# Kernel optimization log

Measured on AMD Instinct MI355X. Metric: run time of the kernel, lower is better.

## Reference

```python
import jax, jax.numpy as jnp
import numpy as np

SIGMA = 1.0
B, M, D = 32, 4, 196608  # groups, matrix_size, flattened feature dim (3*256*256)


def _mmd_kernel_mean(x, y, w):
    # x, y: [B, m, D] float32; w: [B]
    # Faithful to kernel_fn: dist = sqrt(clamp(sum((x-y)^2), 1e-12)) / D / sigma
    # Pairwise squared distances via gram expansion (avoids materializing [B,m,m,D]).
    xn = jnp.sum(x * x, axis=-1)                     # [B, m]
    yn = jnp.sum(y * y, axis=-1)                     # [B, m]
    xy = jnp.einsum('bid,bjd->bij', x, y)            # [B, m, m]
    d2 = jnp.maximum(xn[:, :, None] + yn[:, None, :] - 2.0 * xy, 1e-12)
    denom = float(D) if D > 0 else 1.0
    sigma = max(float(SIGMA), 1e-6)
    dist = jnp.sqrt(d2) / denom / sigma              # [B, m, m]
    expo = jnp.clip(-dist * w[:, None, None], -1e6, 0.0)
    k = jnp.nan_to_num(jnp.exp(expo), nan=0.0, posinf=0.0, neginf=0.0)
    return jnp.nan_to_num(jnp.mean(k, axis=(1, 2)), nan=0.0)  # [B]


def setup_inputs() -> dict:
    key = jax.random.key(0)
    k1, k2, k3, k4 = jax.random.split(key, 4)
    return {
        'f_st': jax.random.normal(k1, (B, M, D), dtype=jnp.float32),
        'f_sr': jax.random.normal(k2, (B, M, D), dtype=jnp.float32),
        'wt': jax.random.uniform(k3, (B,), dtype=jnp.float32),
        'wtout': jax.random.uniform(k4, (B,), dtype=jnp.float32),
    }


def reference(f_st, f_sr, wt, wtout):
    f_st = f_st.astype(jnp.float32)
    f_sr = f_sr.astype(jnp.float32)
    inter_sample = _mmd_kernel_mean(f_st, f_st, wt)
    inter_gt = _mmd_kernel_mean(f_sr, f_sr, wt)
    cross = _mmd_kernel_mean(f_st, f_sr, wt)
    loss_raw = jnp.nan_to_num(inter_sample + inter_gt - 2.0 * cross, nan=0.0)
    loss = jnp.nan_to_num(wtout * loss_raw, nan=0.0)
    return jnp.mean(loss)
```

## Files before the change

kernel.cpp:

```cpp
#include <hip/hip_runtime.h>


constexpr int NB = 32;
constexpr int MM = 4;
constexpr int DD = 196608;
constexpr int D4 = DD / 4;
constexpr int BPG = 24;
constexpr int NTHREADS = 256;
constexpr int TB = 128;
constexpr int CHUNK4 = D4 / BPG;
constexpr int NITER = CHUNK4 / TB;
constexpr int NBUF = 3;
constexpr int NPAIR = 18;
constexpr int NACC = 36;

__device__ __forceinline__ void gl_lds16(const float4* gsrc, float4* lds_dst) {
    __builtin_amdgcn_global_load_lds(
        (const __attribute__((address_space(1))) void*)gsrc,
        (__attribute__((address_space(3))) void*)lds_dst,
        16, 0, 0);
}

__device__ __forceinline__ float dot4(const float4& a, const float4& b) {
    return a.x * b.x + a.y * b.y + a.z * b.z + a.w * b.w;
}

__global__ __launch_bounds__(NTHREADS) void mmd_partial_kernel(
    const float* __restrict__ st, const float* __restrict__ sr,
    float* __restrict__ partial)
{
    __shared__ float4 buf[NBUF][8][TB];
    __shared__ float red[4][NPAIR];

    const int b    = blockIdx.x / BPG;
    const int blk  = blockIdx.x % BPG;
    const int c0   = blk * CHUNK4;
    const int tid  = threadIdx.x;
    const int wave = tid >> 6;
    const int lane = tid & 63;
    const int col  = tid & (TB - 1);
    const int set  = wave >> 1;

    const float4* stb = reinterpret_cast<const float4*>(st) + (size_t)b * MM * D4;
    const float4* srb = reinterpret_cast<const float4*>(sr) + (size_t)b * MM * D4;

    const int r0 = 2 * wave;
    const float4* g0 = (r0 < 4 ? stb + (size_t)r0 * D4
                                : srb + (size_t)(r0 - 4) * D4) + c0 + lane;
    const float4* g1 = (r0 + 1 < 4 ? stb + (size_t)(r0 + 1) * D4
                                    : srb + (size_t)(r0 - 3) * D4) + c0 + lane;

    auto stage = [&](int s) {
        const int m   = s % NBUF;
        const int off = s * TB;
        gl_lds16(g0 + off,      &buf[m][r0][0]);
        gl_lds16(g0 + off + 64, &buf[m][r0][64]);
        gl_lds16(g1 + off,      &buf[m][r0 + 1][0]);
        gl_lds16(g1 + off + 64, &buf[m][r0 + 1][64]);
    };

    float acc[NPAIR];
#pragma unroll
    for (int k = 0; k < NPAIR; ++k) acc[k] = 0.0f;

    stage(0);
    stage(1);

#pragma unroll
    for (int t = 0; t < NITER; ++t) {
        asm volatile("s_waitcnt lgkmcnt(0)" ::: "memory");
        if (t == NITER - 1) asm volatile("s_waitcnt vmcnt(0)" ::: "memory");
        else                asm volatile("s_waitcnt vmcnt(4)" ::: "memory");
        __builtin_amdgcn_s_barrier();
        if (t + 2 < NITER) stage(t + 2);

        const int m = t % NBUF;
        float4 x[8];
#pragma unroll
        for (int r = 0; r < 8; ++r) x[r] = buf[m][r][col];

        if (set == 0) {
            int a = 0;
#pragma unroll
            for (int i = 0; i < MM; ++i)
#pragma unroll
                for (int j = i; j < MM; ++j) { acc[a] += dot4(x[i], x[j]); ++a; }
#pragma unroll
            for (int i = 0; i < 2; ++i)
#pragma unroll
                for (int j = 0; j < MM; ++j) { acc[a] += dot4(x[i], x[4 + j]); ++a; }
        } else {
            int a = 0;
#pragma unroll
            for (int i = 0; i < MM; ++i)
#pragma unroll
                for (int j = i; j < MM; ++j) { acc[a] += dot4(x[4 + i], x[4 + j]); ++a; }
#pragma unroll
            for (int i = 2; i < 4; ++i)
#pragma unroll
                for (int j = 0; j < MM; ++j) { acc[a] += dot4(x[i], x[4 + j]); ++a; }
        }
    }

#pragma unroll
    for (int k = 0; k < NPAIR; ++k) {
        float v = acc[k];
        for (int off = 32; off > 0; off >>= 1) v += __shfl_down(v, off, 64);
        acc[k] = v;
    }
    if (lane == 0) {
#pragma unroll
        for (int k = 0; k < NPAIR; ++k) red[wave][k] = acc[k];
    }
    __syncthreads();

    if (tid < NACC) {
        const int k = tid;
        float v;
        if (k < 10)       v = red[0][k]      + red[1][k];
        else if (k < 20)  v = red[2][k - 10] + red[3][k - 10];
        else if (k < 28)  v = red[0][10 + (k - 20)] + red[1][10 + (k - 20)];
        else              v = red[2][10 + (k - 28)] + red[3][10 + (k - 28)];
        partial[(size_t)blockIdx.x * NACC + k] = v;
    }
}

__global__ __launch_bounds__(1024) void mmd_final_kernel(
    const float* __restrict__ partial, const float* __restrict__ wt,
    const float* __restrict__ wtout, float* __restrict__ out)
{
    __shared__ float acc_s[NB][NACC];
    for (int p = threadIdx.x; p < NB * NACC; p += 1024) {
        const int b = p / NACC;
        const int k = p % NACC;
        float s = 0.0f;
        for (int blk = 0; blk < BPG; ++blk)
            s += partial[((size_t)b * BPG + blk) * NACC + k];
        acc_s[b][k] = s;
    }
    __syncthreads();

    __shared__ float lds[NB];
    const int b = threadIdx.x;
    if (b < NB) {
        const float* a = acc_s[b];
        float ss[MM][MM], rr[MM][MM], sg[MM][MM];
        {
            int k = 0;
            for (int i = 0; i < MM; ++i)
                for (int j = i; j < MM; ++j) { ss[i][j] = a[k]; ss[j][i] = a[k]; ++k; }
            for (int i = 0; i < MM; ++i)
                for (int j = i; j < MM; ++j) { rr[i][j] = a[k]; rr[j][i] = a[k]; ++k; }
            for (int i = 0; i < MM; ++i)
                for (int j = 0; j < MM; ++j) { sg[i][j] = a[k]; ++k; }
        }

        const float w    = wt[b];
        const float invD = 1.0f / (float)DD;
        auto kv = [&](float d2) -> float {
            d2 = fmaxf(d2, 1e-12f);
            float dist = sqrtf(d2) * invD;
            float e = -dist * w;
            e = fminf(fmaxf(e, -1e6f), 0.0f);
            return expf(e);
        };

        float mss = 0.0f, mrr = 0.0f, msr = 0.0f;
        for (int i = 0; i < MM; ++i) {
            for (int j = 0; j < MM; ++j) {
                mss += kv(ss[i][i] + ss[j][j] - 2.0f * ss[i][j]);
                mrr += kv(rr[i][i] + rr[j][j] - 2.0f * rr[i][j]);
                msr += kv(ss[i][i] + rr[j][j] - 2.0f * sg[i][j]);
            }
        }
        const float inv16 = 1.0f / 16.0f;
        float loss_raw = mss * inv16 + mrr * inv16 - 2.0f * (msr * inv16);
        lds[b] = wtout[b] * loss_raw;
    }
    __syncthreads();
    if (threadIdx.x == 0) {
        float s = 0.0f;
        for (int i = 0; i < NB; ++i) s += lds[i];
        out[0] = s / (float)NB;
    }
}

extern "C" void kernel_launch(void* const* d_in, const int* in_sizes, int n_in,
                              void* d_out, int out_size, void* d_ws, size_t ws_size,
                              hipStream_t stream) {
    const float* f_st  = (const float*)d_in[0];
    const float* f_sr  = (const float*)d_in[1];
    const float* wt    = (const float*)d_in[2];
    const float* wtout = (const float*)d_in[3];
    float* out     = (float*)d_out;
    float* partial = (float*)d_ws;

    mmd_partial_kernel<<<NB * BPG, NTHREADS, 0, stream>>>(f_st, f_sr, partial);
    mmd_final_kernel<<<1, 1024, 0, stream>>>(partial, wt, wtout, out);
}
```

Before: 43.21 us.

## Fuse final reduction via last-block atomics, double grid, rebalance per-wave work

Merges the partial and final kernels into one launch. Per-group atomic counters let the last finishing block of each group reduce its partials, and a global counter lets the last group write the output. The grid grows to 48 blocks per group with a 64-wide tile, and work is repartitioned so each wave owns a distinct Gram sub-block: st-st, sr-sr, or half of the cross terms. The goal is to remove the second kernel launch, its serialized tail and the redundant LDS reads. The cost is an extra memset launch, atomic traffic, and a per-wave work imbalance of 10 vs 8 dot products.

```diff
diff --git a/kernel.cpp b/kernel.cpp
--- a/kernel.cpp
+++ b/kernel.cpp
@@ -5,14 +5,19 @@
 constexpr int MM = 4;
 constexpr int DD = 196608;
 constexpr int D4 = DD / 4;
-constexpr int BPG = 24;
+constexpr int BPG = 48;
+constexpr int NBLOCKS = NB * BPG;
 constexpr int NTHREADS = 256;
-constexpr int TB = 128;
+constexpr int TB = 64;
 constexpr int CHUNK4 = D4 / BPG;
 constexpr int NITER = CHUNK4 / TB;
 constexpr int NBUF = 3;
-constexpr int NPAIR = 18;
 constexpr int NACC = 36;
+
+constexpr size_t PART_BYTES = (size_t)NBLOCKS * NACC * 4;
+constexpr size_t GCNT_OFF   = PART_BYTES;
+constexpr size_t FCNT_OFF   = GCNT_OFF + 128;
+constexpr size_t GLOSS_OFF  = GCNT_OFF + 256;
 
 __device__ __forceinline__ void gl_lds16(const float4* gsrc, float4* lds_dst) {
     __builtin_amdgcn_global_load_lds(
@@ -25,12 +30,24 @@
     return a.x * b.x + a.y * b.y + a.z * b.z + a.w * b.w;
 }
 
-__global__ __launch_bounds__(NTHREADS) void mmd_partial_kernel(
+__device__ __forceinline__ void st_agent(float* p, float v) {
+    __hip_atomic_store(p, v, __ATOMIC_RELAXED, __HIP_MEMORY_SCOPE_AGENT);
+}
+__device__ __forceinline__ float ld_agent(const float* p) {
+    return __hip_atomic_load(p, __ATOMIC_RELAXED, __HIP_MEMORY_SCOPE_AGENT);
+}
+
+__global__ __launch_bounds__(NTHREADS, 6) void mmd_fused_kernel(
     const float* __restrict__ st, const float* __restrict__ sr,
-    float* __restrict__ partial)
+    const float* __restrict__ wt, const float* __restrict__ wtout,
+    float* __restrict__ partial, int* __restrict__ gcnt,
+    int* __restrict__ fcnt, float* __restrict__ gloss,
+    float* __restrict__ out)
 {
     __shared__ float4 buf[NBUF][8][TB];
-    __shared__ float red[4][NPAIR];
+    __shared__ float red[4][10];
+    __shared__ float sgrp[NACC];
+    __shared__ int s_flag;
 
     const int b    = blockIdx.x / BPG;
     const int blk  = blockIdx.x % BPG;
@@ -38,8 +55,6 @@
     const int tid  = threadIdx.x;
     const int wave = tid >> 6;
     const int lane = tid & 63;
-    const int col  = tid & (TB - 1);
-    const int set  = wave >> 1;
 
     const float4* stb = reinterpret_cast<const float4*>(st) + (size_t)b * MM * D4;
     const float4* srb = reinterpret_cast<const float4*>(sr) + (size_t)b * MM * D4;
@@ -51,17 +66,14 @@
                                     : srb + (size_t)(r0 - 3) * D4) + c0 + lane;
 
     auto stage = [&](int s) {
-        const int m   = s % NBUF;
-        const int off = s * TB;
-        gl_lds16(g0 + off,      &buf[m][r0][0]);
-        gl_lds16(g0 + off + 64, &buf[m][r0][64]);
-        gl_lds16(g1 + off,      &buf[m][r0 + 1][0]);
-        gl_lds16(g1 + off + 64, &buf[m][r0 + 1][64]);
+        const int m = s % NBUF;
+        gl_lds16(g0 + s * TB, &buf[m][r0][0]);
+        gl_lds16(g1 + s * TB, &buf[m][r0 + 1][0]);
     };
 
-    float acc[NPAIR];
-#pragma unroll
-    for (int k = 0; k < NPAIR; ++k) acc[k] = 0.0f;
+    float acc[10];
+#pragma unroll
+    for (int k = 0; k < 10; ++k) acc[k] = 0.0f;
 
     stage(0);
     stage(1);
@@ -70,80 +82,86 @@
     for (int t = 0; t < NITER; ++t) {
         asm volatile("s_waitcnt lgkmcnt(0)" ::: "memory");
         if (t == NITER - 1) asm volatile("s_waitcnt vmcnt(0)" ::: "memory");
-        else                asm volatile("s_waitcnt vmcnt(4)" ::: "memory");
+        else                asm volatile("s_waitcnt vmcnt(2)" ::: "memory");
         __builtin_amdgcn_s_barrier();
         if (t + 2 < NITER) stage(t + 2);
 
         const int m = t % NBUF;
-        float4 x[8];
-#pragma unroll
-        for (int r = 0; r < 8; ++r) x[r] = buf[m][r][col];
-
-        if (set == 0) {
+        if (wave == 0) {
+            float4 x[4];
+#pragma unroll
+            for (int r = 0; r < 4; ++r) x[r] = buf[m][r][lane];
             int a = 0;
 #pragma unroll
             for (int i = 0; i < MM; ++i)
 #pragma unroll
                 for (int j = i; j < MM; ++j) { acc[a] += dot4(x[i], x[j]); ++a; }
+        } else if (wave == 1) {
+            float4 x[4];
+#pragma unroll
+            for (int r = 0; r < 4; ++r) x[r] = buf[m][4 + r][lane];
+            int a = 0;
+#pragma unroll
+            for (int i = 0; i < MM; ++i)
+#pragma unroll
+                for (int j = i; j < MM; ++j) { acc[a] += dot4(x[i], x[j]); ++a; }
+        } else {
+            const int ib = (wave == 2) ? 0 : 2;
+            float4 xi[2], y[4];
+            xi[0] = buf[m][ib][lane];
+            xi[1] = buf[m][ib + 1][lane];
+#pragma unroll
+            for (int j = 0; j < 4; ++j) y[j] = buf[m][4 + j][lane];
+            int a = 0;
 #pragma unroll
             for (int i = 0; i < 2; ++i)
 #pragma unroll
-                for (int j = 0; j < MM; ++j) { acc[a] += dot4(x[i], x[4 + j]); ++a; }
-        } else {
-            int a = 0;
-#pragma unroll
-            for (int i = 0; i < MM; ++i)
-#pragma unroll
-                for (int j = i; j < MM; ++j) { acc[a] += dot4(x[4 + i], x[4 + j]); ++a; }
-#pragma unroll
-            for (int i = 2; i < 4; ++i)
-#pragma unroll
-                for (int j = 0; j < MM; ++j) { acc[a] += dot4(x[i], x[4 + j]); ++a; }
-        }
-    }
-
-#pragma unroll
-    for (int k = 0; k < NPAIR; ++k) {
+                for (int j = 0; j < 4; ++j) { acc[a] += dot4(xi[i], y[j]); ++a; }
+        }
+    }
+
+#pragma unroll
+    for (int k = 0; k < 10; ++k) {
         float v = acc[k];
         for (int off = 32; off > 0; off >>= 1) v += __shfl_down(v, off, 64);
         acc[k] = v;
     }
     if (lane == 0) {
 #pragma unroll
-        for (int k = 0; k < NPAIR; ++k) red[wave][k] = acc[k];
+        for (int k = 0; k < 10; ++k) red[wave][k] = acc[k];
     }
     __syncthreads();
 
     if (tid < NACC) {
         const int k = tid;
         float v;
-        if (k < 10)       v = red[0][k]      + red[1][k];
-        else if (k < 20)  v = red[2][k - 10] + red[3][k - 10];
-        else if (k < 28)  v = red[0][10 + (k - 20)] + red[1][10 + (k - 20)];
-        else              v = red[2][10 + (k - 28)] + red[3][10 + (k - 28)];
-        partial[(size_t)blockIdx.x * NACC + k] = v;
-    }
-}
-
-__global__ __launch_bounds__(1024) void mmd_final_kernel(
-    const float* __restrict__ partial, const float* __restrict__ wt,
-    const float* __restrict__ wtout, float* __restrict__ out)
-{
-    __shared__ float acc_s[NB][NACC];
-    for (int p = threadIdx.x; p < NB * NACC; p += 1024) {
-        const int b = p / NACC;
-        const int k = p % NACC;
+        if (k < 10)      v = red[0][k];
+        else if (k < 20) v = red[1][k - 10];
+        else if (k < 28) v = red[2][k - 20];
+        else             v = red[3][k - 28];
+        st_agent(&partial[(size_t)blockIdx.x * NACC + k], v);
+    }
+    __syncthreads();
+
+    if (tid == 0) {
+        int old = __hip_atomic_fetch_add(&gcnt[b], 1, __ATOMIC_ACQ_REL,
+                                         __HIP_MEMORY_SCOPE_AGENT);
+        s_flag = (old == BPG - 1);
+    }
+    __syncthreads();
+    if (!s_flag) return;
+
+    if (tid < NACC) {
         float s = 0.0f;
-        for (int blk = 0; blk < BPG; ++blk)
-            s += partial[((size_t)b * BPG + blk) * NACC + k];
-        acc_s[b][k] = s;
-    }
-    __syncthreads();
-
-    __shared__ float lds[NB];
-    const int b = threadIdx.x;
-    if (b < NB) {
-        const float* a = acc_s[b];
+        const float* p = partial + (size_t)b * BPG * NACC + tid;
+#pragma unroll
+        for (int q = 0; q < BPG; ++q) s += ld_agent(p + q * NACC);
+        sgrp[tid] = s;
+    }
+    __syncthreads();
+
+    if (tid == 0) {
+        const float* a = sgrp;
         float ss[MM][MM], rr[MM][MM], sg[MM][MM];
         {
             int k = 0;
@@ -154,7 +172,6 @@
             for (int i = 0; i < MM; ++i)
                 for (int j = 0; j < MM; ++j) { sg[i][j] = a[k]; ++k; }
         }
-
         const float w    = wt[b];
         const float invD = 1.0f / (float)DD;
         auto kv = [&](float d2) -> float {
@@ -164,7 +181,6 @@
             e = fminf(fmaxf(e, -1e6f), 0.0f);
             return expf(e);
         };
-
         float mss = 0.0f, mrr = 0.0f, msr = 0.0f;
         for (int i = 0; i < MM; ++i) {
             for (int j = 0; j < MM; ++j) {
@@ -175,13 +191,15 @@
         }
         const float inv16 = 1.0f / 16.0f;
         float loss_raw = mss * inv16 + mrr * inv16 - 2.0f * (msr * inv16);
-        lds[b] = wtout[b] * loss_raw;
-    }
-    __syncthreads();
-    if (threadIdx.x == 0) {
-        float s = 0.0f;
-        for (int i = 0; i < NB; ++i) s += lds[i];
-        out[0] = s / (float)NB;
+        st_agent(&gloss[b], wtout[b] * loss_raw);
+
+        int old2 = __hip_atomic_fetch_add(fcnt, 1, __ATOMIC_ACQ_REL,
+                                          __HIP_MEMORY_SCOPE_AGENT);
+        if (old2 == NB - 1) {
+            float s = 0.0f;
+            for (int i = 0; i < NB; ++i) s += ld_agent(&gloss[i]);
+            out[0] = s / (float)NB;
+        }
     }
 }
 
@@ -194,7 +212,12 @@
     const float* wtout = (const float*)d_in[3];
     float* out     = (float*)d_out;
     float* partial = (float*)d_ws;
-
-    mmd_partial_kernel<<<NB * BPG, NTHREADS, 0, stream>>>(f_st, f_sr, partial);
-    mmd_final_kernel<<<1, 1024, 0, stream>>>(partial, wt, wtout, out);
-}
+    int*   gcnt    = (int*)((char*)d_ws + GCNT_OFF);
+    int*   fcnt    = (int*)((char*)d_ws + FCNT_OFF);
+    float* gloss   = (float*)((char*)d_ws + GLOSS_OFF);
+
+    hipMemsetAsync((char*)d_ws + GCNT_OFF, 0, 256, stream);
+
+    mmd_fused_kernel<<<NBLOCKS, NTHREADS, 0, stream>>>(
+        f_st, f_sr, wt, wtout, partial, gcnt, fcnt, gloss, out);
+}
```

After: 84.74 us. +96.1%, slower.

## Split pair work by wave and double block count with smaller tiles

Applied to the files above, without the earlier changes.

Each wave now owns one class of dot products (st-st, sr-sr, or half of the cross terms) over all 64 lanes, instead of two wave-sets each covering half the columns. Each wave therefore reads only 4-6 rows from LDS rather than 8 and keeps 10 accumulators instead of 18, which lowers LDS traffic and register use. The tile width is halved and blocks per group doubled, with an occupancy hint of 6 blocks per CU, to put more loads in flight on this memory-bound reduction. In exchange the per-wave work is uneven (the cross-term waves do 8 dot products against 10 for the others) and more partial results must be summed in the final kernel.

```diff
diff --git a/kernel.cpp b/kernel.cpp
--- a/kernel.cpp
+++ b/kernel.cpp
@@ -5,13 +5,12 @@
 constexpr int MM = 4;
 constexpr int DD = 196608;
 constexpr int D4 = DD / 4;
-constexpr int BPG = 24;
+constexpr int BPG = 48;
 constexpr int NTHREADS = 256;
-constexpr int TB = 128;
+constexpr int TB = 64;
 constexpr int CHUNK4 = D4 / BPG;
 constexpr int NITER = CHUNK4 / TB;
 constexpr int NBUF = 3;
-constexpr int NPAIR = 18;
 constexpr int NACC = 36;
 
 __device__ __forceinline__ void gl_lds16(const float4* gsrc, float4* lds_dst) {
@@ -25,12 +24,12 @@
     return a.x * b.x + a.y * b.y + a.z * b.z + a.w * b.w;
 }
 
-__global__ __launch_bounds__(NTHREADS) void mmd_partial_kernel(
+__global__ __launch_bounds__(NTHREADS, 6) void mmd_partial_kernel(
     const float* __restrict__ st, const float* __restrict__ sr,
     float* __restrict__ partial)
 {
     __shared__ float4 buf[NBUF][8][TB];
-    __shared__ float red[4][NPAIR];
+    __shared__ float red[4][10];
 
     const int b    = blockIdx.x / BPG;
     const int blk  = blockIdx.x % BPG;
@@ -38,8 +37,6 @@
     const int tid  = threadIdx.x;
     const int wave = tid >> 6;
     const int lane = tid & 63;
-    const int col  = tid & (TB - 1);
-    const int set  = wave >> 1;
 
     const float4* stb = reinterpret_cast<const float4*>(st) + (size_t)b * MM * D4;
     const float4* srb = reinterpret_cast<const float4*>(sr) + (size_t)b * MM * D4;
@@ -51,17 +48,14 @@
                                     : srb + (size_t)(r0 - 3) * D4) + c0 + lane;
 
     auto stage = [&](int s) {
-        const int m   = s % NBUF;
-        const int off = s * TB;
-        gl_lds16(g0 + off,      &buf[m][r0][0]);
-        gl_lds16(g0 + off + 64, &buf[m][r0][64]);
-        gl_lds16(g1 + off,      &buf[m][r0 + 1][0]);
-        gl_lds16(g1 + off + 64, &buf[m][r0 + 1][64]);
+        const int m = s % NBUF;
+        gl_lds16(g0 + s * TB, &buf[m][r0][0]);
+        gl_lds16(g1 + s * TB, &buf[m][r0 + 1][0]);
     };
 
-    float acc[NPAIR];
-#pragma unroll
-    for (int k = 0; k < NPAIR; ++k) acc[k] = 0.0f;
+    float acc[10];
+#pragma unroll
+    for (int k = 0; k < 10; ++k) acc[k] = 0.0f;
 
     stage(0);
     stage(1);
@@ -70,57 +64,63 @@
     for (int t = 0; t < NITER; ++t) {
         asm volatile("s_waitcnt lgkmcnt(0)" ::: "memory");
         if (t == NITER - 1) asm volatile("s_waitcnt vmcnt(0)" ::: "memory");
-        else                asm volatile("s_waitcnt vmcnt(4)" ::: "memory");
+        else                asm volatile("s_waitcnt vmcnt(2)" ::: "memory");
         __builtin_amdgcn_s_barrier();
         if (t + 2 < NITER) stage(t + 2);
 
         const int m = t % NBUF;
-        float4 x[8];
-#pragma unroll
-        for (int r = 0; r < 8; ++r) x[r] = buf[m][r][col];
-
-        if (set == 0) {
+        if (wave == 0) {
+            float4 x[4];
+#pragma unroll
+            for (int r = 0; r < 4; ++r) x[r] = buf[m][r][lane];
             int a = 0;
 #pragma unroll
             for (int i = 0; i < MM; ++i)
 #pragma unroll
                 for (int j = i; j < MM; ++j) { acc[a] += dot4(x[i], x[j]); ++a; }
+        } else if (wave == 1) {
+            float4 x[4];
+#pragma unroll
+            for (int r = 0; r < 4; ++r) x[r] = buf[m][4 + r][lane];
+            int a = 0;
+#pragma unroll
+            for (int i = 0; i < MM; ++i)
+#pragma unroll
+                for (int j = i; j < MM; ++j) { acc[a] += dot4(x[i], x[j]); ++a; }
+        } else {
+            const int ib = (wave == 2) ? 0 : 2;
+            float4 xi[2], y[4];
+            xi[0] = buf[m][ib][lane];
+            xi[1] = buf[m][ib + 1][lane];
+#pragma unroll
+            for (int j = 0; j < 4; ++j) y[j] = buf[m][4 + j][lane];
+            int a = 0;
 #pragma unroll
             for (int i = 0; i < 2; ++i)
 #pragma unroll
-                for (int j = 0; j < MM; ++j) { acc[a] += dot4(x[i], x[4 + j]); ++a; }
-        } else {
-            int a = 0;
-#pragma unroll
-            for (int i = 0; i < MM; ++i)
-#pragma unroll
-                for (int j = i; j < MM; ++j) { acc[a] += dot4(x[4 + i], x[4 + j]); ++a; }
-#pragma unroll
-            for (int i = 2; i < 4; ++i)
-#pragma unroll
-                for (int j = 0; j < MM; ++j) { acc[a] += dot4(x[i], x[4 + j]); ++a; }
+                for (int j = 0; j < 4; ++j) { acc[a] += dot4(xi[i], y[j]); ++a; }
         }
     }
 
 #pragma unroll
-    for (int k = 0; k < NPAIR; ++k) {
+    for (int k = 0; k < 10; ++k) {
         float v = acc[k];
         for (int off = 32; off > 0; off >>= 1) v += __shfl_down(v, off, 64);
         acc[k] = v;
     }
     if (lane == 0) {
 #pragma unroll
-        for (int k = 0; k < NPAIR; ++k) red[wave][k] = acc[k];
+        for (int k = 0; k < 10; ++k) red[wave][k] = acc[k];
     }
     __syncthreads();
 
     if (tid < NACC) {
         const int k = tid;
         float v;
-        if (k < 10)       v = red[0][k]      + red[1][k];
-        else if (k < 20)  v = red[2][k - 10] + red[3][k - 10];
-        else if (k < 28)  v = red[0][10 + (k - 20)] + red[1][10 + (k - 20)];
-        else              v = red[2][10 + (k - 28)] + red[3][10 + (k - 28)];
+        if (k < 10)      v = red[0][k];
+        else if (k < 20) v = red[1][k - 10];
+        else if (k < 28) v = red[2][k - 20];
+        else             v = red[3][k - 28];
         partial[(size_t)blockIdx.x * NACC + k] = v;
     }
 }
```

Measured after the change: 68.54 us. 1.59x slower.
